# Kernel optimization log

Hardware: AMD Instinct MI355X
Metric: run time of the kernel (lower is better)

## Reference

```python
import jax, jax.numpy as jnp
import numpy as np

N = 1024      # num_nodes
D = 64        # node_embedding_dim
H = 64        # hidden_dim
LN_EPS = 1e-5


def setup_inputs() -> dict:
    key = jax.random.key(0)
    ks = jax.random.split(key, 6)
    node_embeddings = jax.random.normal(ks[0], (N, D), dtype=jnp.float32)
    valid_mask = jax.random.randint(ks[1], (N * N,), 0, 2).astype(jnp.float32)
    s1 = 1.0 / np.sqrt(2 * D)
    s2 = 1.0 / np.sqrt(H)
    W1 = jax.random.normal(ks[2], (2 * D, H), dtype=jnp.float32) * s1
    b1 = jnp.zeros((H,), jnp.float32)
    g1 = jnp.ones((H,), jnp.float32)
    be1 = jnp.zeros((H,), jnp.float32)
    W2 = jax.random.normal(ks[3], (H, H), dtype=jnp.float32) * s2
    b2 = jnp.zeros((H,), jnp.float32)
    g2 = jnp.ones((H,), jnp.float32)
    be2 = jnp.zeros((H,), jnp.float32)
    W3 = jax.random.normal(ks[4], (H, 1), dtype=jnp.float32) * s2
    b3 = jnp.zeros((1,), jnp.float32)
    return {
        "node_embeddings": node_embeddings, "valid_mask": valid_mask,
        "W1": W1, "b1": b1, "g1": g1, "be1": be1,
        "W2": W2, "b2": b2, "g2": g2, "be2": be2,
        "W3": W3, "b3": b3,
    }


def _layer_norm(x, g, b):
    m = jnp.mean(x, axis=-1, keepdims=True)
    v = jnp.mean((x - m) ** 2, axis=-1, keepdims=True)
    return (x - m) * jax.lax.rsqrt(v + LN_EPS) * g + b


def reference(node_embeddings, valid_mask, W1, b1, g1, be1, W2, b2, g2, be2, W3, b3):
    n, d = node_embeddings.shape
    # Build all ordered pairs (i, j): concat([emb_i, emb_j]) -> [n*n, 2d]
    src = jnp.broadcast_to(node_embeddings[:, None, :], (n, n, d))
    tgt = jnp.broadcast_to(node_embeddings[None, :, :], (n, n, d))
    e = jnp.concatenate([src, tgt], axis=-1).reshape(n * n, 2 * d)
    # MLP: Linear -> LayerNorm -> ReLU (x2 hidden) -> Linear(1)
    h = jax.nn.relu(_layer_norm(e @ W1 + b1, g1, be1))
    h = jax.nn.relu(_layer_norm(h @ W2 + b2, g2, be2))
    scores = (h @ W3 + b3)[:, 0]  # [n*n]
    # Original never scores self-edges (i == j) and multiplies by valid_mask.
    off_diag = 1.0 - jnp.eye(n, dtype=scores.dtype).reshape(-1)
    return scores * valid_mask * off_diag
```

## Files before the change

### kernel.cpp

```cpp
#include <hip/hip_runtime.h>
#include <hip/hip_bf16.h>

#define NN 1024
#define LN_EPS 1e-5f

typedef __bf16 bf16x8 __attribute__((ext_vector_type(8)));
typedef float floatx4 __attribute__((ext_vector_type(4)));
typedef float floatx2 __attribute__((ext_vector_type(2)));

__global__ void precompute_ab(const float* __restrict__ emb, const float* __restrict__ W1,
                              const float* __restrict__ b1, const float* __restrict__ W2,
                              float* __restrict__ Ap, float* __restrict__ Bt,
                              float* __restrict__ sumA, float* __restrict__ sumB,
                              __bf16* __restrict__ Wf) {
    if (blockIdx.x == 1024) {
        int lane = threadIdx.x;
        int m_l = lane & 15, kg = lane >> 4;
#pragma unroll
        for (int mt = 0; mt < 4; mt++)
#pragma unroll
            for (int kc = 0; kc < 2; kc++) {
                bf16x8 f;
#pragma unroll
                for (int t = 0; t < 8; t++) {
                    int k = kc * 32 + kg * 8 + t;
                    f[t] = (__bf16)W2[k * 64 + mt * 16 + m_l];
                }
                *(bf16x8*)&Wf[((mt * 2 + kc) * 64 + lane) * 8] = f;
            }
        return;
    }
    __shared__ __align__(16) float e[64];
    int i = blockIdx.x, h = threadIdx.x;
    e[h] = emb[i * 64 + h];
    __syncthreads();
    float a = b1[h], b = 0.f;
#pragma unroll
    for (int d = 0; d < 64; d++) {
        a = fmaf(e[d], W1[d * 64 + h], a);
        b = fmaf(e[d], W1[(64 + d) * 64 + h], b);
    }
    Ap[i * 64 + h] = a;
    Bt[h * NN + i] = b;
    float ra = a, rb = b;
#pragma unroll
    for (int off = 1; off < 64; off <<= 1) {
        ra += __shfl_xor(ra, off);
        rb += __shfl_xor(rb, off);
    }
    if (h == 0) { sumA[i] = ra; sumB[i] = rb; }
}

__global__ __launch_bounds__(256, 4) void fused(
    const float* __restrict__ Ap, const float* __restrict__ Bt, const __bf16* __restrict__ Wf,
    const float* __restrict__ sumA, const float* __restrict__ sumB,
    const float* __restrict__ g1, const float* __restrict__ be1, const float* __restrict__ b2,
    const float* __restrict__ g2, const float* __restrict__ be2, const float* __restrict__ W3,
    const float* __restrict__ b3, const float* __restrict__ mask, float* __restrict__ out) {
    __shared__ __align__(16) float Arow[64], G1[64], BE1[64], B2s[64], G2s[64], BE2s[64], W3s[64];
    __shared__ __align__(16) __bf16 h1t[4][64 * 64];

    int tid = threadIdx.x;
    int wave = tid >> 6, lane = tid & 63;
    int i = blockIdx.x >> 2;
    int j0 = (blockIdx.x & 3) * 256 + wave * 64;

    if (tid < 64) {
        Arow[tid] = Ap[i * 64 + tid];
        G1[tid] = g1[tid];  BE1[tid] = be1[tid];
        B2s[tid] = b2[tid]; G2s[tid] = g2[tid]; BE2s[tid] = be2[tid];
        W3s[tid] = W3[tid];
    }
    __syncthreads();

    int m_l = lane & 15, kg = lane >> 4;

    bf16x8 afrag[4][2];
#pragma unroll
    for (int mt = 0; mt < 4; mt++)
#pragma unroll
        for (int kc = 0; kc < 2; kc++)
            afrag[mt][kc] = *(const bf16x8*)&Wf[((mt * 2 + kc) * 64 + lane) * 8];

    float sBj = sumB[j0 + lane];
    const float* btp = Bt + j0 + lane;
    floatx2 x2[32];
    floatx2 qa = {0.f, 0.f}, qb = {0.f, 0.f};
#pragma unroll
    for (int h2 = 0; h2 < 32; h2++) {
        floatx2 bb = { btp[(2 * h2) * NN], btp[(2 * h2 + 1) * NN] };
        floatx2 aa = *(const floatx2*)&Arow[2 * h2];
        floatx2 v = aa + bb;
        x2[h2] = v;
        if (h2 & 1) qb += v * v;
        else        qa += v * v;
    }
    floatx2 qs = qa + qb;
    float sq = qs[0] + qs[1];
    float m1 = (sumA[i] + sBj) * 0.015625f;
    float var1 = fmaf(m1, -m1, sq * 0.015625f);
    float rs1 = rsqrtf(var1 + LN_EPS);
    floatx2 p1 = {rs1, rs1};
    float ofs = -m1 * rs1;
    floatx2 o1 = {ofs, ofs};

    __bf16* rowp = &h1t[wave][lane * 64];
    int sw = lane & 7;
#pragma unroll
    for (int c = 0; c < 8; c++) {
        bf16x8 fr;
#pragma unroll
        for (int t = 0; t < 4; t++) {
            floatx2 gg = *(const floatx2*)&G1[c * 8 + 2 * t];
            floatx2 ee = *(const floatx2*)&BE1[c * 8 + 2 * t];
            floatx2 xn = x2[c * 4 + t] * p1 + o1;
            floatx2 y  = xn * gg + ee;
            y = __builtin_elementwise_max(y, (floatx2){0.f, 0.f});
            fr[2 * t]     = (__bf16)y[0];
            fr[2 * t + 1] = (__bf16)y[1];
        }
        *(bf16x8*)(rowp + ((c ^ sw) * 8)) = fr;
    }
    asm volatile("s_waitcnt lgkmcnt(0)" ::: "memory");

    floatx4 acc[4][4];
#pragma unroll
    for (int a = 0; a < 4; a++)
#pragma unroll
        for (int b = 0; b < 4; b++) acc[a][b] = (floatx4){0.f, 0.f, 0.f, 0.f};

    const __bf16* wbase = &h1t[wave][0];
#pragma unroll
    for (int nt = 0; nt < 4; nt++) {
        int pair = nt * 16 + m_l;
#pragma unroll
        for (int kc = 0; kc < 2; kc++) {
            int chunk = kc * 4 + kg;
            bf16x8 bfrag = *(const bf16x8*)(wbase + pair * 64 + ((chunk ^ (pair & 7)) * 8));
#pragma unroll
            for (int mt = 0; mt < 4; mt++)
                acc[mt][nt] =
                    __builtin_amdgcn_mfma_f32_16x16x32_bf16(afrag[mt][kc], bfrag, acc[mt][nt], 0, 0, 0);
        }
    }

    float b3v = b3[0];

#pragma unroll
    for (int nt = 0; nt < 4; nt++) {
        floatx2 s2v = {0.f, 0.f}, q2v = {0.f, 0.f};
#pragma unroll
        for (int mt = 0; mt < 4; mt++) {
            floatx2 blo = *(const floatx2*)&B2s[mt * 16 + kg * 4];
            floatx2 bhi = *(const floatx2*)&B2s[mt * 16 + kg * 4 + 2];
            floatx2 vlo = { acc[mt][nt][0], acc[mt][nt][1] };
            floatx2 vhi = { acc[mt][nt][2], acc[mt][nt][3] };
            vlo += blo; vhi += bhi;
            acc[mt][nt][0] = vlo[0]; acc[mt][nt][1] = vlo[1];
            acc[mt][nt][2] = vhi[0]; acc[mt][nt][3] = vhi[1];
            s2v += vlo; s2v += vhi;
            q2v += vlo * vlo; q2v += vhi * vhi;
        }
        float s2 = s2v[0] + s2v[1];
        float q2 = q2v[0] + q2v[1];
        s2 += __shfl_xor(s2, 16); s2 += __shfl_xor(s2, 32);
        q2 += __shfl_xor(q2, 16); q2 += __shfl_xor(q2, 32);
        float m2 = s2 * 0.015625f;
        float var2 = fmaf(m2, -m2, q2 * 0.015625f);
        float rs2 = rsqrtf(var2 + LN_EPS);
        floatx2 p2 = {rs2, rs2};
        float o2s = -m2 * rs2;
        floatx2 o2 = {o2s, o2s};

        floatx2 scv = {0.f, 0.f};
#pragma unroll
        for (int mt = 0; mt < 4; mt++) {
#pragma unroll
            for (int hh = 0; hh < 2; hh++) {
                floatx2 g = *(const floatx2*)&G2s[mt * 16 + kg * 4 + 2 * hh];
                floatx2 e = *(const floatx2*)&BE2s[mt * 16 + kg * 4 + 2 * hh];
                floatx2 w = *(const floatx2*)&W3s[mt * 16 + kg * 4 + 2 * hh];
                floatx2 v = { acc[mt][nt][2 * hh], acc[mt][nt][2 * hh + 1] };
                floatx2 xn = v * p2 + o2;
                floatx2 y  = xn * g + e;
                y = __builtin_elementwise_max(y, (floatx2){0.f, 0.f});
                scv += y * w;
            }
        }
        float sc = scv[0] + scv[1];
        sc += __shfl_xor(sc, 16); sc += __shfl_xor(sc, 32);

        if (kg == 0) {
            int j = j0 + nt * 16 + m_l;
            int p = i * NN + j;
            out[p] = (i == j) ? 0.f : (sc + b3v) * mask[p];
        }
    }
}

extern "C" void kernel_launch(void* const* d_in, const int* in_sizes, int n_in,
                              void* d_out, int out_size, void* d_ws, size_t ws_size,
                              hipStream_t stream) {
    const float* emb = (const float*)d_in[0];
    const float* mask = (const float*)d_in[1];
    const float* W1 = (const float*)d_in[2];
    const float* b1 = (const float*)d_in[3];
    const float* g1 = (const float*)d_in[4];
    const float* be1 = (const float*)d_in[5];
    const float* W2 = (const float*)d_in[6];
    const float* b2 = (const float*)d_in[7];
    const float* g2 = (const float*)d_in[8];
    const float* be2 = (const float*)d_in[9];
    const float* W3 = (const float*)d_in[10];
    const float* b3 = (const float*)d_in[11];
    float* out = (float*)d_out;

    float* Ap = (float*)d_ws;
    float* Bt = Ap + 1024 * 64;
    float* sA = Bt + 64 * 1024;
    float* sB = sA + 1024;
    __bf16* Wf = (__bf16*)(sB + 1024);

    precompute_ab<<<1025, 64, 0, stream>>>(emb, W1, b1, W2, Ap, Bt, sA, sB, Wf);
    fused<<<4096, 256, 0, stream>>>(Ap, Bt, Wf, sA, sB, g1, be1, b2, g2, be2, W3, b3, mask, out);
}
```

Baseline: 113.8 us.

## Compute LN1 variance via MFMA cross-term dot product and interleave Bt layout

The first LayerNorm's sum of squares is now expanded as |a|^2 + |b|^2 + 2 a·b. The norms are precomputed per node and the cross term comes from bf16 MFMA, so the separate pass that kept all 64 pre-activation values in registers goes away. Bt is stored in a 4-wide interleaved layout so that each pass can use float4 loads. The b2 bias is folded into the accumulator init, and the LN2/W3 parameters are hoisted into registers. The bf16 cross term loses precision in the variance, which can suffer cancellation when the variance is small.

```diff
diff --git a/kernel.cpp b/kernel.cpp
--- a/kernel.cpp
+++ b/kernel.cpp
@@ -8,10 +8,14 @@
 typedef float floatx4 __attribute__((ext_vector_type(4)));
 typedef float floatx2 __attribute__((ext_vector_type(2)));
 
+__device__ __forceinline__ floatx4 splat4(float s) { return (floatx4){s, s, s, s}; }
+
 __global__ void precompute_ab(const float* __restrict__ emb, const float* __restrict__ W1,
                               const float* __restrict__ b1, const float* __restrict__ W2,
-                              float* __restrict__ Ap, float* __restrict__ Bt,
+                              float* __restrict__ Ap, float* __restrict__ Bt4,
+                              __bf16* __restrict__ Abf, __bf16* __restrict__ Bbf,
                               float* __restrict__ sumA, float* __restrict__ sumB,
+                              float* __restrict__ sumA2, float* __restrict__ sumB2,
                               __bf16* __restrict__ Wf) {
     if (blockIdx.x == 1024) {
         int lane = threadIdx.x;
@@ -41,19 +45,26 @@
         b = fmaf(e[d], W1[(64 + d) * 64 + h], b);
     }
     Ap[i * 64 + h] = a;
-    Bt[h * NN + i] = b;
-    float ra = a, rb = b;
+    Abf[i * 64 + h] = (__bf16)a;
+    Bt4[(h >> 2) * 4096 + i * 4 + (h & 3)] = b;
+    Bbf[i * 64 + h] = (__bf16)b;
+    float ra = a, rb = b, ra2 = a * a, rb2 = b * b;
 #pragma unroll
     for (int off = 1; off < 64; off <<= 1) {
         ra += __shfl_xor(ra, off);
         rb += __shfl_xor(rb, off);
-    }
-    if (h == 0) { sumA[i] = ra; sumB[i] = rb; }
+        ra2 += __shfl_xor(ra2, off);
+        rb2 += __shfl_xor(rb2, off);
+    }
+    if (h == 0) { sumA[i] = ra; sumB[i] = rb; sumA2[i] = ra2; sumB2[i] = rb2; }
 }
 
 __global__ __launch_bounds__(256, 4) void fused(
-    const float* __restrict__ Ap, const float* __restrict__ Bt, const __bf16* __restrict__ Wf,
+    const float* __restrict__ Ap, const float* __restrict__ Bt4,
+    const __bf16* __restrict__ Abf, const __bf16* __restrict__ Bbf,
+    const __bf16* __restrict__ Wf,
     const float* __restrict__ sumA, const float* __restrict__ sumB,
+    const float* __restrict__ sumA2, const float* __restrict__ sumB2,
     const float* __restrict__ g1, const float* __restrict__ be1, const float* __restrict__ b2,
     const float* __restrict__ g2, const float* __restrict__ be2, const float* __restrict__ W3,
     const float* __restrict__ b3, const float* __restrict__ mask, float* __restrict__ out) {
@@ -75,6 +86,27 @@
 
     int m_l = lane & 15, kg = lane >> 4;
 
+    bf16x8 afA0 = *(const bf16x8*)&Abf[i * 64 + kg * 8];
+    bf16x8 afA1 = *(const bf16x8*)&Abf[i * 64 + 32 + kg * 8];
+    floatx4 xacc[4];
+#pragma unroll
+    for (int nt = 0; nt < 4; nt++) xacc[nt] = splat4(0.f);
+#pragma unroll
+    for (int nt = 0; nt < 4; nt++) {
+        const __bf16* bp = &Bbf[(j0 + nt * 16 + m_l) * 64 + kg * 8];
+        xacc[nt] = __builtin_amdgcn_mfma_f32_16x16x32_bf16(afA0, *(const bf16x8*)bp, xacc[nt], 0, 0, 0);
+        xacc[nt] = __builtin_amdgcn_mfma_f32_16x16x32_bf16(afA1, *(const bf16x8*)(bp + 32), xacc[nt], 0, 0, 0);
+    }
+    float c0 = (kg & 2) ? xacc[2][0] : xacc[0][0];
+    float c1 = (kg & 2) ? xacc[3][0] : xacc[1][0];
+    float cross = (kg & 1) ? c1 : c0;
+
+    float m1 = (sumA[i] + sumB[j0 + lane]) * 0.015625f;
+    float sq = fmaf(2.f, cross, sumA2[i] + sumB2[j0 + lane]);
+    float var1 = fmaf(m1, -m1, sq * 0.015625f);
+    float rs1 = rsqrtf(var1 + LN_EPS);
+    floatx4 RS = splat4(rs1), OF = splat4(-m1 * rs1);
+
     bf16x8 afrag[4][2];
 #pragma unroll
     for (int mt = 0; mt < 4; mt++)
@@ -82,52 +114,38 @@
         for (int kc = 0; kc < 2; kc++)
             afrag[mt][kc] = *(const bf16x8*)&Wf[((mt * 2 + kc) * 64 + lane) * 8];
 
-    float sBj = sumB[j0 + lane];
-    const float* btp = Bt + j0 + lane;
-    floatx2 x2[32];
-    floatx2 qa = {0.f, 0.f}, qb = {0.f, 0.f};
-#pragma unroll
-    for (int h2 = 0; h2 < 32; h2++) {
-        floatx2 bb = { btp[(2 * h2) * NN], btp[(2 * h2 + 1) * NN] };
-        floatx2 aa = *(const floatx2*)&Arow[2 * h2];
-        floatx2 v = aa + bb;
-        x2[h2] = v;
-        if (h2 & 1) qb += v * v;
-        else        qa += v * v;
-    }
-    floatx2 qs = qa + qb;
-    float sq = qs[0] + qs[1];
-    float m1 = (sumA[i] + sBj) * 0.015625f;
-    float var1 = fmaf(m1, -m1, sq * 0.015625f);
-    float rs1 = rsqrtf(var1 + LN_EPS);
-    floatx2 p1 = {rs1, rs1};
-    float ofs = -m1 * rs1;
-    floatx2 o1 = {ofs, ofs};
-
     __bf16* rowp = &h1t[wave][lane * 64];
     int sw = lane & 7;
+    const float* btp = Bt4 + (j0 + lane) * 4;
 #pragma unroll
     for (int c = 0; c < 8; c++) {
+        floatx4 bb0 = *(const floatx4*)(btp + (2 * c) * 4096);
+        floatx4 bb1 = *(const floatx4*)(btp + (2 * c + 1) * 4096);
+        floatx4 a0 = *(const floatx4*)&Arow[c * 8];
+        floatx4 a1 = *(const floatx4*)&Arow[c * 8 + 4];
+        floatx4 gg0 = *(const floatx4*)&G1[c * 8];
+        floatx4 gg1 = *(const floatx4*)&G1[c * 8 + 4];
+        floatx4 ee0 = *(const floatx4*)&BE1[c * 8];
+        floatx4 ee1 = *(const floatx4*)&BE1[c * 8 + 4];
+        floatx4 y0 = ((a0 + bb0) * RS + OF) * gg0 + ee0;
+        floatx4 y1 = ((a1 + bb1) * RS + OF) * gg1 + ee1;
+        y0 = __builtin_elementwise_max(y0, splat4(0.f));
+        y1 = __builtin_elementwise_max(y1, splat4(0.f));
         bf16x8 fr;
-#pragma unroll
-        for (int t = 0; t < 4; t++) {
-            floatx2 gg = *(const floatx2*)&G1[c * 8 + 2 * t];
-            floatx2 ee = *(const floatx2*)&BE1[c * 8 + 2 * t];
-            floatx2 xn = x2[c * 4 + t] * p1 + o1;
-            floatx2 y  = xn * gg + ee;
-            y = __builtin_elementwise_max(y, (floatx2){0.f, 0.f});
-            fr[2 * t]     = (__bf16)y[0];
-            fr[2 * t + 1] = (__bf16)y[1];
-        }
+        fr[0] = (__bf16)y0[0]; fr[1] = (__bf16)y0[1]; fr[2] = (__bf16)y0[2]; fr[3] = (__bf16)y0[3];
+        fr[4] = (__bf16)y1[0]; fr[5] = (__bf16)y1[1]; fr[6] = (__bf16)y1[2]; fr[7] = (__bf16)y1[3];
         *(bf16x8*)(rowp + ((c ^ sw) * 8)) = fr;
     }
     asm volatile("s_waitcnt lgkmcnt(0)" ::: "memory");
 
+    floatx4 b2r[4];
+#pragma unroll
+    for (int mt = 0; mt < 4; mt++) b2r[mt] = *(const floatx4*)&B2s[mt * 16 + kg * 4];
     floatx4 acc[4][4];
 #pragma unroll
-    for (int a = 0; a < 4; a++)
-#pragma unroll
-        for (int b = 0; b < 4; b++) acc[a][b] = (floatx4){0.f, 0.f, 0.f, 0.f};
+    for (int mt = 0; mt < 4; mt++)
+#pragma unroll
+        for (int nt = 0; nt < 4; nt++) acc[mt][nt] = b2r[mt];
 
     const __bf16* wbase = &h1t[wave][0];
 #pragma unroll
@@ -144,6 +162,13 @@
         }
     }
 
+    floatx4 g2r[4], e2r[4], w3r[4];
+#pragma unroll
+    for (int mt = 0; mt < 4; mt++) {
+        g2r[mt] = *(const floatx4*)&G2s[mt * 16 + kg * 4];
+        e2r[mt] = *(const floatx4*)&BE2s[mt * 16 + kg * 4];
+        w3r[mt] = *(const floatx4*)&W3s[mt * 16 + kg * 4];
+    }
     float b3v = b3[0];
 
 #pragma unroll
@@ -151,13 +176,8 @@
         floatx2 s2v = {0.f, 0.f}, q2v = {0.f, 0.f};
 #pragma unroll
         for (int mt = 0; mt < 4; mt++) {
-            floatx2 blo = *(const floatx2*)&B2s[mt * 16 + kg * 4];
-            floatx2 bhi = *(const floatx2*)&B2s[mt * 16 + kg * 4 + 2];
-            floatx2 vlo = { acc[mt][nt][0], acc[mt][nt][1] };
-            floatx2 vhi = { acc[mt][nt][2], acc[mt][nt][3] };
-            vlo += blo; vhi += bhi;
-            acc[mt][nt][0] = vlo[0]; acc[mt][nt][1] = vlo[1];
-            acc[mt][nt][2] = vhi[0]; acc[mt][nt][3] = vhi[1];
+            floatx2 vlo = {acc[mt][nt][0], acc[mt][nt][1]};
+            floatx2 vhi = {acc[mt][nt][2], acc[mt][nt][3]};
             s2v += vlo; s2v += vhi;
             q2v += vlo * vlo; q2v += vhi * vhi;
         }
@@ -166,23 +186,21 @@
         s2 += __shfl_xor(s2, 16); s2 += __shfl_xor(s2, 32);
         q2 += __shfl_xor(q2, 16); q2 += __shfl_xor(q2, 32);
         float m2 = s2 * 0.015625f;
-        float var2 = fmaf(m2, -m2, q2 * 0.015625f);
-        float rs2 = rsqrtf(var2 + LN_EPS);
-        floatx2 p2 = {rs2, rs2};
+        float rs2 = rsqrtf(fmaf(m2, -m2, q2 * 0.015625f) + LN_EPS);
+        floatx2 P2 = {rs2, rs2};
         float o2s = -m2 * rs2;
-        floatx2 o2 = {o2s, o2s};
+        floatx2 O2 = {o2s, o2s};
 
         floatx2 scv = {0.f, 0.f};
 #pragma unroll
         for (int mt = 0; mt < 4; mt++) {
 #pragma unroll
             for (int hh = 0; hh < 2; hh++) {
-                floatx2 g = *(const floatx2*)&G2s[mt * 16 + kg * 4 + 2 * hh];
-                floatx2 e = *(const floatx2*)&BE2s[mt * 16 + kg * 4 + 2 * hh];
-                floatx2 w = *(const floatx2*)&W3s[mt * 16 + kg * 4 + 2 * hh];
-                floatx2 v = { acc[mt][nt][2 * hh], acc[mt][nt][2 * hh + 1] };
-                floatx2 xn = v * p2 + o2;
-                floatx2 y  = xn * g + e;
+                floatx2 v = {acc[mt][nt][2 * hh], acc[mt][nt][2 * hh + 1]};
+                floatx2 g = {g2r[mt][2 * hh], g2r[mt][2 * hh + 1]};
+                floatx2 e = {e2r[mt][2 * hh], e2r[mt][2 * hh + 1]};
+                floatx2 w = {w3r[mt][2 * hh], w3r[mt][2 * hh + 1]};
+                floatx2 y = (v * P2 + O2) * g + e;
                 y = __builtin_elementwise_max(y, (floatx2){0.f, 0.f});
                 scv += y * w;
             }
@@ -216,11 +234,16 @@
     float* out = (float*)d_out;
 
     float* Ap = (float*)d_ws;
-    float* Bt = Ap + 1024 * 64;
-    float* sA = Bt + 64 * 1024;
+    float* Bt4 = Ap + 65536;
+    float* sA = Bt4 + 65536;
     float* sB = sA + 1024;
-    __bf16* Wf = (__bf16*)(sB + 1024);
-
-    precompute_ab<<<1025, 64, 0, stream>>>(emb, W1, b1, W2, Ap, Bt, sA, sB, Wf);
-    fused<<<4096, 256, 0, stream>>>(Ap, Bt, Wf, sA, sB, g1, be1, b2, g2, be2, W3, b3, mask, out);
+    float* sA2 = sB + 1024;
+    float* sB2 = sA2 + 1024;
+    __bf16* Abf = (__bf16*)(sB2 + 1024);
+    __bf16* Bbf = Abf + 65536;
+    __bf16* Wf = Bbf + 65536;
+
+    precompute_ab<<<1025, 64, 0, stream>>>(emb, W1, b1, W2, Ap, Bt4, Abf, Bbf, sA, sB, sA2, sB2, Wf);
+    fused<<<4096, 256, 0, stream>>>(Ap, Bt4, Abf, Bbf, Wf, sA, sB, sA2, sB2,
+                                    g1, be1, b2, g2, be2, W3, b3, mask, out);
 }
```

After: 119.7 us. 5.2% more time.
